# Kernel tuning notes

Hardware: AMD Instinct MI355X
Metric: run time of the kernel (lower is better)

The kernel has to match this reference:

```python
import jax, jax.numpy as jnp
import numpy as np

D_MODEL = 1024
NUM_HEADS = 16
D_HEAD = D_MODEL // NUM_HEADS


def setup_inputs() -> dict:
    key = jax.random.key(0)
    ks = jax.random.split(key, 7)
    B, S = 2, 2048
    scale = 1.0 / np.sqrt(D_MODEL)
    return {
        "x": jax.random.normal(ks[0], (B, S, D_MODEL), dtype=jnp.float32),
        "attn_weights": jnp.zeros((1,), dtype=jnp.float32),  # unused in original forward
        "Wq": jax.random.normal(ks[1], (D_MODEL, D_MODEL), dtype=jnp.float32) * scale,
        "Wk": jax.random.normal(ks[2], (D_MODEL, D_MODEL), dtype=jnp.float32) * scale,
        "Wv": jax.random.normal(ks[3], (D_MODEL, D_MODEL), dtype=jnp.float32) * scale,
        "Wp": jax.random.normal(ks[4], (D_MODEL, D_MODEL), dtype=jnp.float32) * scale,
        "bp": jnp.zeros((D_MODEL,), dtype=jnp.float32),
    }


def reference(x, attn_weights, Wq, Wk, Wv, Wp, bp):
    B, S, D = x.shape
    H, Dh = NUM_HEADS, D_HEAD
    # torch Linear: y = x @ W.T  (weights stored [out, in])
    q = (x @ Wq.T).reshape(B, S, H, Dh).transpose(0, 2, 1, 3)  # [B,H,S,Dh]
    k = (x @ Wk.T).reshape(B, S, H, Dh).transpose(0, 2, 1, 3)
    v = (x @ Wv.T).reshape(B, S, H, Dh).transpose(0, 2, 1, 3)
    # NOTE: original module applies NO 1/sqrt(d) scaling
    scores = jnp.einsum("bhqd,bhkd->bhqk", q, k)
    weights = jax.nn.softmax(scores, axis=-1)  # dropout is inference no-op
    out = jnp.einsum("bhqk,bhkd->bhqd", weights, v)
    out = out.transpose(0, 2, 1, 3).reshape(B, S, D)
    return out @ Wp.T + bp
```

## Files before the change

kernel.cpp:

```cpp
#include <hip/hip_runtime.h>
#include <hip/hip_bf16.h>

#define D_MODEL 1024
#define NUM_HEADS 16
#define D_HEAD 64
#define BATCH 2
#define SEQ 2048
#define TOKENS (BATCH * SEQ)

typedef __attribute__((ext_vector_type(8))) short bf16x8;
typedef __attribute__((ext_vector_type(4))) float f32x4;
typedef __attribute__((ext_vector_type(2))) unsigned int uint2v;

typedef __attribute__((address_space(1))) const unsigned int as1_uint;
typedef __attribute__((address_space(3))) unsigned int as3_uint;

#define LOG2E 1.44269504088896340736f

static __device__ __forceinline__ unsigned short f2bf(float f) {
    unsigned int u = __builtin_bit_cast(unsigned int, f);
    u += 0x7fffu + ((u >> 16) & 1u);
    return (unsigned short)(u >> 16);
}

static __device__ __forceinline__ unsigned int pk2bf(float a, float b) {
    __hip_bfloat162 h = __float22bfloat162_rn(float2{a, b});
    unsigned int u;
    __builtin_memcpy(&u, &h, 4);
    return u;
}

static __device__ __forceinline__ float fast_exp2(float x) {
    return __builtin_amdgcn_exp2f(x);
}

__global__ __launch_bounds__(256) void convert_w(
    const float* __restrict__ Wq, const float* __restrict__ Wk,
    const float* __restrict__ Wv, const float* __restrict__ Wp,
    unsigned short* __restrict__ Wqb, unsigned short* __restrict__ Wkb,
    unsigned short* __restrict__ Wvb, unsigned short* __restrict__ Wpb)
{
    int v = blockIdx.x * 256 + threadIdx.x;
    int w = v >> 18;
    int off = v & ((1 << 18) - 1);
    const float* s = (w == 0) ? Wq : (w == 1) ? Wk : (w == 2) ? Wv : Wp;
    unsigned short* d = (w == 0) ? Wqb : (w == 1) ? Wkb : (w == 2) ? Wvb : Wpb;
    float4 f = ((const float4*)s)[off];
    ushort4 o = { f2bf(f.x), f2bf(f.y), f2bf(f.z), f2bf(f.w) };
    ((ushort4*)d)[off] = o;
}

__global__ __launch_bounds__(512, 4) void qkv_gemm(
    const float* __restrict__ x,
    const unsigned short* __restrict__ Wqb, const unsigned short* __restrict__ Wkb,
    const unsigned short* __restrict__ Wvb,
    unsigned short* __restrict__ Q, unsigned short* __restrict__ Kb,
    unsigned short* __restrict__ Vt)
{
    const int m0 = blockIdx.x * 128;
    const int n0 = blockIdx.y * 64;

    __shared__ __attribute__((aligned(16))) unsigned short sm[40960];

    const int t = threadIdx.x;
    const int wave = t >> 6, lane = t & 63;
    const int wm = (wave & 1) * 64, wn = (wave >> 1) * 16;
    const int l15 = lane & 15, quad = lane >> 4;
    const int sw = l15 & 7;

    const unsigned short* Wz[3] = { Wqb, Wkb, Wvb };

    f32x4 acc[3][4];
#pragma unroll
    for (int z = 0; z < 3; z++)
#pragma unroll
        for (int i = 0; i < 4; i++) acc[z][i] = (f32x4)0.f;

    auto stageW = [&](int k0, int buf) {
        int row = t >> 3, cp = t & 7;
        int c = cp ^ (row & 7);
        int fbase = wave * 64;
#pragma unroll
        for (int z = 0; z < 3; z++)
            __builtin_amdgcn_global_load_lds(
                (as1_uint*)&Wz[z][(size_t)(n0 + row) * D_MODEL + k0 + c * 8],
                (as3_uint*)&sm[buf * 20480 + 8192 + z * 4096 + fbase * 8],
                16, 0, 0);
    };

    float4 ar[2][2];
    auto loadA = [&](int k0) {
#pragma unroll
        for (int i = 0; i < 2; i++) {
            int f = wave * 64 + i * 512 + lane;
            int row = f >> 3, cp = f & 7;
            int c = cp ^ (row & 7);
            const float4* p = (const float4*)&x[(size_t)(m0 + row) * D_MODEL + k0 + c * 8];
            ar[i][0] = p[0];
            ar[i][1] = p[1];
        }
    };
    auto writeA = [&](int buf) {
#pragma unroll
        for (int i = 0; i < 2; i++) {
            int f = wave * 64 + i * 512 + lane;
            union { unsigned short s[8]; uint4 v; } u;
            u.s[0] = f2bf(ar[i][0].x); u.s[1] = f2bf(ar[i][0].y);
            u.s[2] = f2bf(ar[i][0].z); u.s[3] = f2bf(ar[i][0].w);
            u.s[4] = f2bf(ar[i][1].x); u.s[5] = f2bf(ar[i][1].y);
            u.s[6] = f2bf(ar[i][1].z); u.s[7] = f2bf(ar[i][1].w);
            *(uint4*)&sm[buf * 20480 + f * 8] = u.v;
        }
    };

    loadA(0);
    stageW(0, 0);
    writeA(0);
    __syncthreads();

    int cur = 0;
    for (int k0 = 0; k0 < D_MODEL; k0 += 64) {
        bool more = (k0 + 64 < D_MODEL);
        if (more) { stageW(k0 + 64, cur ^ 1); loadA(k0 + 64); }

        const unsigned short* lA = &sm[cur * 20480];
#pragma unroll
        for (int kk = 0; kk < 2; kk++) {
            const int cc = ((kk * 4 + quad) ^ sw) * 8;
            bf16x8 a[4];
#pragma unroll
            for (int mt = 0; mt < 4; mt++)
                a[mt] = *(const bf16x8*)&lA[(wm + mt * 16 + l15) * 64 + cc];
#pragma unroll
            for (int z = 0; z < 3; z++) {
                const unsigned short* lB = &sm[cur * 20480 + 8192 + z * 4096];
                bf16x8 b = *(const bf16x8*)&lB[(wn + l15) * 64 + cc];
#pragma unroll
                for (int mt = 0; mt < 4; mt++)
                    acc[z][mt] = __builtin_amdgcn_mfma_f32_16x16x32_bf16(
                        a[mt], b, acc[z][mt], 0, 0, 0);
            }
        }
        if (more) writeA(cur ^ 1);
        __syncthreads();
        cur ^= 1;
    }

#pragma unroll
    for (int mt = 0; mt < 4; mt++)
#pragma unroll
        for (int r = 0; r < 4; r++) {
            int row = m0 + wm + mt * 16 + quad * 4 + r;
            int col = n0 + wn + l15;
            Q[(size_t)row * D_MODEL + col]  = f2bf(acc[0][mt][r] * LOG2E);
            Kb[(size_t)row * D_MODEL + col] = f2bf(acc[1][mt][r]);
        }
    {
        const int b = m0 >> 11;
        const int srow = (m0 & 2047) + wm + quad * 4;
        const int h = n0 >> 6;
        const int dh = wn + l15;
#pragma unroll
        for (int mt = 0; mt < 4; mt++) {
            ushort4 pk = { f2bf(acc[2][mt][0]), f2bf(acc[2][mt][1]),
                           f2bf(acc[2][mt][2]), f2bf(acc[2][mt][3]) };
            *(ushort4*)&Vt[(size_t)((b * 16 + h) * 64 + dh) * SEQ + srow + mt * 16] = pk;
        }
    }
}

__global__ __launch_bounds__(512, 4) void attn(
    const unsigned short* __restrict__ Q, const unsigned short* __restrict__ K,
    const unsigned short* __restrict__ Vt, unsigned short* __restrict__ O)
{
    const int q0 = blockIdx.y * 128;
    const int bh = blockIdx.x;
    const int b = bh >> 4, h = bh & 15;
    const size_t base = (size_t)b * SEQ * D_MODEL + (size_t)h * D_HEAD;
    const size_t baseV = (size_t)bh * D_HEAD * SEQ;

    __shared__ __attribute__((aligned(16))) char smem[65536];
    unsigned short* lds = (unsigned short*)smem;

    const int t = threadIdx.x;
    const int wave = t >> 6, lane = t & 63;
    const int l15 = lane & 15, quad = lane >> 4;
    const int wq = wave & 3;
    const int sh = wave >> 2;
    const int qw = q0 + wq * 32;
    const int sbase = sh * (SEQ / 2);

    bf16x8 ones;
#pragma unroll
    for (int i = 0; i < 8; i++) ones[i] = (short)0x3F80;

    bf16x8 bq[2][2];
#pragma unroll
    for (int mq = 0; mq < 2; mq++)
#pragma unroll
        for (int kk = 0; kk < 2; kk++)
            bq[mq][kk] = *(const bf16x8*)&Q[base +
                (size_t)(qw + mq * 16 + l15) * D_MODEL + kk * 32 + quad * 8];

    const int tl = t & 255;
    const int sw = l15 & 7;

    auto stage = [&](int soff, int buf) {
#pragma unroll
        for (int i = 0; i < 2; i++) {
            int f = tl + i * 256;
            int row = f >> 3;
            int c = (f & 7) ^ (row & 7);
            __builtin_amdgcn_global_load_lds(
                (as1_uint*)&K[base + (size_t)(sbase + soff + row) * D_MODEL + c * 8],
                (as3_uint*)&lds[buf * 16384 + sh * 4096 + f * 8], 16, 0, 0);
            __builtin_amdgcn_global_load_lds(
                (as1_uint*)&Vt[baseV + (size_t)row * SEQ + sbase + soff + c * 8],
                (as3_uint*)&lds[8192 + buf * 16384 + sh * 4096 + f * 8], 16, 0, 0);
        }
    };

    f32x4 o_acc[2][4];
#pragma unroll
    for (int i = 0; i < 2; i++)
#pragma unroll
        for (int j = 0; j < 4; j++) o_acc[i][j] = (f32x4)0.f;
    f32x4 o_l[2];
#pragma unroll
    for (int i = 0; i < 2; i++) o_l[i] = (f32x4)0.f;

    stage(0, 0);
    __syncthreads();

    int cur = 0;
    for (int s0 = 0; s0 < SEQ / 2; s0 += 64) {
        if (s0 + 64 < SEQ / 2) stage(s0 + 64, cur ^ 1);

        const unsigned short* lK  = lds + cur * 16384 + sh * 4096;
        const unsigned short* lVt = lds + 8192 + cur * 16384 + sh * 4096;

        f32x4 st[4][2];
#pragma unroll
        for (int mt = 0; mt < 4; mt++)
#pragma unroll
            for (int mq = 0; mq < 2; mq++) st[mt][mq] = (f32x4)0.f;
#pragma unroll
        for (int kk = 0; kk < 2; kk++) {
            const int cc = ((kk * 4 + quad) ^ sw) * 8;
#pragma unroll
            for (int mt = 0; mt < 4; mt++) {
                bf16x8 ak = *(const bf16x8*)&lK[(mt * 16 + l15) * 64 + cc];
#pragma unroll
                for (int mq = 0; mq < 2; mq++)
                    st[mt][mq] = __builtin_amdgcn_mfma_f32_16x16x32_bf16(
                        ak, bq[mq][kk], st[mt][mq], 0, 0, 0);
            }
        }

#pragma unroll
        for (int mq = 0; mq < 2; mq++)
#pragma unroll
            for (int mt = 0; mt < 4; mt++)
#pragma unroll
                for (int r = 0; r < 4; r++)
                    st[mt][mq][r] = fast_exp2(st[mt][mq][r]);

        bf16x8 pa[2][2];
#pragma unroll
        for (int mq = 0; mq < 2; mq++)
#pragma unroll
            for (int kk = 0; kk < 2; kk++) {
                unsigned int cw[4];
#pragma unroll
                for (int j = 0; j < 2; j++) {
                    unsigned int w0 = pk2bf(st[2 * kk][mq][2 * j],
                                            st[2 * kk][mq][2 * j + 1]);
                    unsigned int w1 = pk2bf(st[2 * kk + 1][mq][2 * j],
                                            st[2 * kk + 1][mq][2 * j + 1]);
                    uint2v uv = __builtin_amdgcn_permlane32_swap(w0, w1, false, false);
                    uint2v f  = __builtin_amdgcn_permlane16_swap(uv[0], uv[1], false, false);
                    cw[j]     = f[0];
                    cw[2 + j] = f[1];
                }
                union { unsigned int w[4]; bf16x8 v; } uu;
                uu.w[0] = cw[0]; uu.w[1] = cw[1]; uu.w[2] = cw[2]; uu.w[3] = cw[3];
                pa[mq][kk] = uu.v;
            }

#pragma unroll
        for (int kk = 0; kk < 2; kk++) {
            const int cc = ((kk * 4 + quad) ^ sw) * 8;
            bf16x8 bv[4];
#pragma unroll
            for (int nt = 0; nt < 4; nt++)
                bv[nt] = *(const bf16x8*)&lVt[(nt * 16 + l15) * 64 + cc];
#pragma unroll
            for (int mq = 0; mq < 2; mq++) {
#pragma unroll
                for (int nt = 0; nt < 4; nt++)
                    o_acc[mq][nt] = __builtin_amdgcn_mfma_f32_16x16x32_bf16(
                        pa[mq][kk], bv[nt], o_acc[mq][nt], 0, 0, 0);
                o_l[mq] = __builtin_amdgcn_mfma_f32_16x16x32_bf16(
                    pa[mq][kk], ones, o_l[mq], 0, 0, 0);
            }
        }
        __syncthreads();
        cur ^= 1;
    }

    float* sO = (float*)&smem[0];
    float* sL = (float*)&smem[36864];
    if (sh == 1) {
#pragma unroll
        for (int mq = 0; mq < 2; mq++) {
#pragma unroll
            for (int r = 0; r < 4; r++)
                sL[wq * 32 + mq * 16 + quad * 4 + r] = o_l[mq][r];
#pragma unroll
            for (int nt = 0; nt < 4; nt++)
#pragma unroll
                for (int r = 0; r < 4; r++)
                    sO[(wq * 32 + mq * 16 + quad * 4 + r) * 68 + nt * 16 + l15] =
                        o_acc[mq][nt][r];
        }
    }
    __syncthreads();
    if (sh == 0) {
#pragma unroll
        for (int mq = 0; mq < 2; mq++) {
            float inv[4];
#pragma unroll
            for (int r = 0; r < 4; r++)
                inv[r] = 1.f / (o_l[mq][r] + sL[wq * 32 + mq * 16 + quad * 4 + r]);
#pragma unroll
            for (int nt = 0; nt < 4; nt++)
#pragma unroll
                for (int r = 0; r < 4; r++) {
                    int row = qw + mq * 16 + quad * 4 + r;
                    float v = o_acc[mq][nt][r] +
                              sO[(wq * 32 + mq * 16 + quad * 4 + r) * 68 + nt * 16 + l15];
                    O[base + (size_t)row * D_MODEL + nt * 16 + l15] = f2bf(v * inv[r]);
                }
        }
    }
}

__global__ __launch_bounds__(512, 4) void proj_gemm(
    const unsigned short* __restrict__ A, const unsigned short* __restrict__ W,
    const float* __restrict__ bias, float* __restrict__ out)
{
    const int m0 = blockIdx.x * 128;
    const int n0 = blockIdx.y * 64;

    __shared__ __attribute__((aligned(16))) unsigned short sm[24576];

    const int t = threadIdx.x;
    const int wave = t >> 6, lane = t & 63;
    const int wm = (wave & 1) * 64, wn = (wave >> 1) * 16;
    const int l15 = lane & 15, quad = lane >> 4;
    const int sw = l15 & 7;

    f32x4 acc[4];
#pragma unroll
    for (int i = 0; i < 4; i++) acc[i] = (f32x4)0.f;

    auto stage = [&](int k0, int buf) {
#pragma unroll
        for (int i = 0; i < 2; i++) {
            int fbase = wave * 64 + i * 512;
            int f = fbase + lane;
            int row = f >> 3, cp = f & 7;
            int c = cp ^ (row & 7);
            __builtin_amdgcn_global_load_lds(
                (as1_uint*)&A[(size_t)(m0 + row) * D_MODEL + k0 + c * 8],
                (as3_uint*)&sm[buf * 12288 + fbase * 8], 16, 0, 0);
        }
        {
            int row = t >> 3, cp = t & 7;
            int c = cp ^ (row & 7);
            int fbase = wave * 64;
            __builtin_amdgcn_global_load_lds(
                (as1_uint*)&W[(size_t)(n0 + row) * D_MODEL + k0 + c * 8],
                (as3_uint*)&sm[buf * 12288 + 8192 + fbase * 8], 16, 0, 0);
        }
    };

    stage(0, 0);
    __syncthreads();

    int cur = 0;
    for (int k0 = 0; k0 < D_MODEL; k0 += 64) {
        if (k0 + 64 < D_MODEL) stage(k0 + 64, cur ^ 1);

        const unsigned short* lA = &sm[cur * 12288];
        const unsigned short* lB = &sm[cur * 12288 + 8192];
#pragma unroll
        for (int kk = 0; kk < 2; kk++) {
            const int cc = ((kk * 4 + quad) ^ sw) * 8;
            bf16x8 a[4];
#pragma unroll
            for (int mt = 0; mt < 4; mt++)
                a[mt] = *(const bf16x8*)&lA[(wm + mt * 16 + l15) * 64 + cc];
            bf16x8 b = *(const bf16x8*)&lB[(wn + l15) * 64 + cc];
#pragma unroll
            for (int mt = 0; mt < 4; mt++)
                acc[mt] = __builtin_amdgcn_mfma_f32_16x16x32_bf16(
                    a[mt], b, acc[mt], 0, 0, 0);
        }
        __syncthreads();
        cur ^= 1;
    }

    const int col = n0 + wn + l15;
    const float bc = bias[col];
#pragma unroll
    for (int mt = 0; mt < 4; mt++)
#pragma unroll
        for (int r = 0; r < 4; r++) {
            int row = m0 + wm + mt * 16 + quad * 4 + r;
            out[(size_t)row * D_MODEL + col] = acc[mt][r] + bc;
        }
}

extern "C" void kernel_launch(void* const* d_in, const int* in_sizes, int n_in,
                              void* d_out, int out_size, void* d_ws, size_t ws_size,
                              hipStream_t stream)
{
    const float* x  = (const float*)d_in[0];
    const float* Wq = (const float*)d_in[2];
    const float* Wk = (const float*)d_in[3];
    const float* Wv = (const float*)d_in[4];
    const float* Wp = (const float*)d_in[5];
    const float* bp = (const float*)d_in[6];
    float* out = (float*)d_out;

    unsigned short* Q   = (unsigned short*)d_ws;
    unsigned short* K   = Q   + (size_t)TOKENS * D_MODEL;
    unsigned short* Vt  = K   + (size_t)TOKENS * D_MODEL;
    unsigned short* O   = Vt  + (size_t)TOKENS * D_MODEL;
    unsigned short* Wqb = O   + (size_t)TOKENS * D_MODEL;
    unsigned short* Wkb = Wqb + (size_t)D_MODEL * D_MODEL;
    unsigned short* Wvb = Wkb + (size_t)D_MODEL * D_MODEL;
    unsigned short* Wpb = Wvb + (size_t)D_MODEL * D_MODEL;

    convert_w<<<4096, 256, 0, stream>>>(Wq, Wk, Wv, Wp,
                                        Wqb, Wkb, Wvb, Wpb);
    qkv_gemm<<<dim3(TOKENS / 128, D_MODEL / 64), 512, 0, stream>>>(
        x, Wqb, Wkb, Wvb, Q, K, Vt);
    attn<<<dim3(BATCH * NUM_HEADS, SEQ / 128), 512, 0, stream>>>(Q, K, Vt, O);
    proj_gemm<<<dim3(TOKENS / 128, D_MODEL / 64), 512, 0, stream>>>(O, Wpb, bp, out);
}
```

Before: 170.2 us.

## Drop split-KV in attention; each 4-wave block sweeps full sequence

The attention kernel previously used 8 waves per block, splitting the key sequence into two halves and merging the partial outputs and row sums through shared memory at the end. Now each block has 4 waves that each own 32 query rows and loop over the full 2048-key sequence, so the LDS merge, the extra barrier and half of the shared memory go away. The launch bounds change to 256 threads with 5 blocks per CU. In exchange there is half as much parallelism inside each block and the per-block loop is twice as long, which may hurt latency hiding.

```diff
diff --git a/kernel.cpp b/kernel.cpp
--- a/kernel.cpp
+++ b/kernel.cpp
@@ -169,7 +169,7 @@
     }
 }
 
-__global__ __launch_bounds__(512, 4) void attn(
+__global__ __launch_bounds__(256, 5) void attn(
     const unsigned short* __restrict__ Q, const unsigned short* __restrict__ K,
     const unsigned short* __restrict__ Vt, unsigned short* __restrict__ O)
 {
@@ -179,16 +179,13 @@
     const size_t base = (size_t)b * SEQ * D_MODEL + (size_t)h * D_HEAD;
     const size_t baseV = (size_t)bh * D_HEAD * SEQ;
 
-    __shared__ __attribute__((aligned(16))) char smem[65536];
+    __shared__ __attribute__((aligned(16))) char smem[32768];
     unsigned short* lds = (unsigned short*)smem;
 
     const int t = threadIdx.x;
     const int wave = t >> 6, lane = t & 63;
     const int l15 = lane & 15, quad = lane >> 4;
-    const int wq = wave & 3;
-    const int sh = wave >> 2;
-    const int qw = q0 + wq * 32;
-    const int sbase = sh * (SEQ / 2);
+    const int qw = q0 + wave * 32;
 
     bf16x8 ones;
 #pragma unroll
@@ -202,21 +199,20 @@
             bq[mq][kk] = *(const bf16x8*)&Q[base +
                 (size_t)(qw + mq * 16 + l15) * D_MODEL + kk * 32 + quad * 8];
 
-    const int tl = t & 255;
     const int sw = l15 & 7;
 
     auto stage = [&](int soff, int buf) {
 #pragma unroll
         for (int i = 0; i < 2; i++) {
-            int f = tl + i * 256;
+            int f = t + i * 256;
             int row = f >> 3;
             int c = (f & 7) ^ (row & 7);
             __builtin_amdgcn_global_load_lds(
-                (as1_uint*)&K[base + (size_t)(sbase + soff + row) * D_MODEL + c * 8],
-                (as3_uint*)&lds[buf * 16384 + sh * 4096 + f * 8], 16, 0, 0);
+                (as1_uint*)&K[base + (size_t)(soff + row) * D_MODEL + c * 8],
+                (as3_uint*)&lds[buf * 8192 + f * 8], 16, 0, 0);
             __builtin_amdgcn_global_load_lds(
-                (as1_uint*)&Vt[baseV + (size_t)row * SEQ + sbase + soff + c * 8],
-                (as3_uint*)&lds[8192 + buf * 16384 + sh * 4096 + f * 8], 16, 0, 0);
+                (as1_uint*)&Vt[baseV + (size_t)row * SEQ + soff + c * 8],
+                (as3_uint*)&lds[4096 + buf * 8192 + f * 8], 16, 0, 0);
         }
     };
 
@@ -233,11 +229,11 @@
     __syncthreads();
 
     int cur = 0;
-    for (int s0 = 0; s0 < SEQ / 2; s0 += 64) {
-        if (s0 + 64 < SEQ / 2) stage(s0 + 64, cur ^ 1);
-
-        const unsigned short* lK  = lds + cur * 16384 + sh * 4096;
-        const unsigned short* lVt = lds + 8192 + cur * 16384 + sh * 4096;
+    for (int s0 = 0; s0 < SEQ; s0 += 64) {
+        if (s0 + 64 < SEQ) stage(s0 + 64, cur ^ 1);
+
+        const unsigned short* lK  = lds + cur * 8192;
+        const unsigned short* lVt = lds + 4096 + cur * 8192;
 
         f32x4 st[4][2];
 #pragma unroll
@@ -308,40 +304,20 @@
         cur ^= 1;
     }
 
-    float* sO = (float*)&smem[0];
-    float* sL = (float*)&smem[36864];
-    if (sh == 1) {
-#pragma unroll
-        for (int mq = 0; mq < 2; mq++) {
-#pragma unroll
-            for (int r = 0; r < 4; r++)
-                sL[wq * 32 + mq * 16 + quad * 4 + r] = o_l[mq][r];
-#pragma unroll
-            for (int nt = 0; nt < 4; nt++)
-#pragma unroll
-                for (int r = 0; r < 4; r++)
-                    sO[(wq * 32 + mq * 16 + quad * 4 + r) * 68 + nt * 16 + l15] =
-                        o_acc[mq][nt][r];
-        }
-    }
-    __syncthreads();
-    if (sh == 0) {
-#pragma unroll
-        for (int mq = 0; mq < 2; mq++) {
-            float inv[4];
-#pragma unroll
-            for (int r = 0; r < 4; r++)
-                inv[r] = 1.f / (o_l[mq][r] + sL[wq * 32 + mq * 16 + quad * 4 + r]);
-#pragma unroll
-            for (int nt = 0; nt < 4; nt++)
-#pragma unroll
-                for (int r = 0; r < 4; r++) {
-                    int row = qw + mq * 16 + quad * 4 + r;
-                    float v = o_acc[mq][nt][r] +
-                              sO[(wq * 32 + mq * 16 + quad * 4 + r) * 68 + nt * 16 + l15];
-                    O[base + (size_t)row * D_MODEL + nt * 16 + l15] = f2bf(v * inv[r]);
-                }
-        }
+#pragma unroll
+    for (int mq = 0; mq < 2; mq++) {
+        float inv[4];
+#pragma unroll
+        for (int r = 0; r < 4; r++)
+            inv[r] = 1.f / o_l[mq][r];
+#pragma unroll
+        for (int nt = 0; nt < 4; nt++)
+#pragma unroll
+            for (int r = 0; r < 4; r++) {
+                int row = qw + mq * 16 + quad * 4 + r;
+                O[base + (size_t)row * D_MODEL + nt * 16 + l15] =
+                    f2bf(o_acc[mq][nt][r] * inv[r]);
+            }
     }
 }
 
@@ -447,6 +423,6 @@
                                         Wqb, Wkb, Wvb, Wpb);
     qkv_gemm<<<dim3(TOKENS / 128, D_MODEL / 64), 512, 0, stream>>>(
         x, Wqb, Wkb, Wvb, Q, K, Vt);
-    attn<<<dim3(BATCH * NUM_HEADS, SEQ / 128), 512, 0, stream>>>(Q, K, Vt, O);
+    attn<<<dim3(BATCH * NUM_HEADS, SEQ / 128), 256, 0, stream>>>(Q, K, Vt, O);
     proj_gemm<<<dim3(TOKENS / 128, D_MODEL / 64), 512, 0, stream>>>(O, Wpb, bp, out);
 }
```

Measured after the change: 199.6 us. 17.2% more time.
